# Kernel tuning notes

Measured on AMD Instinct MI355X. Metric: run time of the kernel, lower is better.

## Reference

```python
import jax, jax.numpy as jnp
import numpy as np

H = 16
DH = 64


def _apply_rotary(x, cos, sin):
    # x: [b, h, s, d]; cos/sin: [s, d//2] -> broadcast to [1, 1, s, d//2]
    x1 = x[..., ::2]
    x2 = x[..., 1::2]
    c = cos[None, None]
    s = sin[None, None]
    rot = jnp.stack([x1 * c - x2 * s, x1 * s + x2 * c], axis=-1)
    return rot.reshape(x.shape)


def setup_inputs() -> dict:
    key = jax.random.key(0)
    ks = jax.random.split(key, 7)
    dim = 1024
    std = 0.02
    x = jax.random.normal(ks[0], (2, 2048, dim), dtype=jnp.float32)
    persistent = jax.random.normal(ks[1], (2, 16, dim), dtype=jnp.float32)
    memory = jax.random.normal(ks[2], (2, 64, dim), dtype=jnp.float32)
    Wq = jax.random.normal(ks[3], (dim, dim), dtype=jnp.float32) * std
    Wk = jax.random.normal(ks[4], (dim, dim), dtype=jnp.float32) * std
    Wv = jax.random.normal(ks[5], (dim, dim), dtype=jnp.float32) * std
    Wo = jax.random.normal(ks[6], (dim, dim), dtype=jnp.float32) * std
    return {"x": x, "persistent": persistent, "memory": memory,
            "Wq": Wq, "Wk": Wk, "Wv": Wv, "Wo": Wo}


def reference(x, persistent, memory, Wq, Wk, Wv, Wo):
    b, L, dim = x.shape
    P = persistent.shape[1] + memory.shape[1]  # prefix_len
    full_x = jnp.concatenate([persistent, memory, x], axis=1)  # [b, P+L, dim]
    S = full_x.shape[1]
    scale = DH ** -0.5

    def proj(W):
        y = full_x @ W.T  # [b, S, dim]
        return y.reshape(b, S, H, DH).transpose(0, 2, 1, 3)  # [b, H, S, DH]

    q = proj(Wq)
    k = proj(Wk)
    v = proj(Wv)

    # RoPE only on the main (input) segment, positions starting at 0.
    pos = jnp.arange(L, dtype=jnp.float32)
    inv_freq = 1.0 / (10000.0 ** (jnp.arange(0, DH, 2, dtype=jnp.float32) / DH))
    freqs = pos[:, None] * inv_freq[None, :]  # [L, DH//2]
    cos, sin = jnp.cos(freqs), jnp.sin(freqs)

    q_main = _apply_rotary(q[:, :, P:], cos, sin)  # [b, H, L, DH]
    k = jnp.concatenate([k[:, :, :P], _apply_rotary(k[:, :, P:], cos, sin)], axis=2)

    # Only main-segment query rows affect the returned output (output[:, P:]).
    # Mask for main queries: prefix keys fully visible; causal within main.
    qi = jnp.arange(L)[:, None]
    kj = jnp.arange(S)[None, :]
    mask = (kj < P) | ((kj - P) <= qi)  # [L, S]

    scores = jnp.einsum('bhqd,bhkd->bhqk', q_main, k) * scale  # [b, H, L, S]
    scores = jnp.where(mask[None, None], scores, -jnp.inf)
    attn = jax.nn.softmax(scores, axis=-1)
    out = jnp.einsum('bhqk,bhkd->bhqd', attn, v)  # [b, H, L, DH]
    out = out.transpose(0, 2, 1, 3).reshape(b, L, dim)
    return out @ Wo.T
```

## Files before the change

### kernel.cpp

```cpp
#include <hip/hip_runtime.h>
#include <math.h>

#define BB    2
#define LL    2048
#define DIM   1024
#define NH    16
#define DHD   64
#define NPER  16
#define NMEM  64
#define PFX   80
#define SS    2128
#define MQKV  (BB*SS)
#define NQKV  3072
#define MOUT  (BB*LL)

typedef __attribute__((ext_vector_type(4)))  float f32x4;
typedef __attribute__((ext_vector_type(16))) float f32x16;
typedef __attribute__((ext_vector_type(8)))  short bf16x8;
typedef unsigned short u16;
typedef unsigned int   u32;

union I4B8 { int4 i; bf16x8 v; };

__device__ __forceinline__ u16 f2bf(float x) {
    union { float f; u32 u; } v; v.f = x;
    return (u16)((v.u + 0x7fffu + ((v.u >> 16) & 1u)) >> 16);
}
__device__ __forceinline__ u32 cvtpk(float lo, float hi) {
    u32 r; asm("v_cvt_pk_bf16_f32 %0, %1, %2" : "=v"(r) : "v"(lo), "v"(hi));
    return r;
}
__device__ __forceinline__ void gload_lds16(const void* g, void* l) {
    __builtin_amdgcn_global_load_lds(
        (__attribute__((address_space(1))) void*)(g),
        (__attribute__((address_space(3))) void*)(l), 16, 0, 0);
}

__global__ __launch_bounds__(256)
void prep_kernel(const float* __restrict__ x,  const float* __restrict__ pe,
                 const float* __restrict__ me, const float* __restrict__ Wq,
                 const float* __restrict__ Wk, const float* __restrict__ Wv,
                 const float* __restrict__ Wo,
                 u16* __restrict__ xbf, u16* __restrict__ wqkv,
                 u16* __restrict__ wobf,
                 float* __restrict__ ropeC, float* __restrict__ ropeS)
{
    const int nthr = gridDim.x * blockDim.x;
    const int t0   = blockIdx.x * blockDim.x + threadIdx.x;

    for (int g = t0; g < MQKV * (DIM / 4); g += nthr) {
        int d4  = g & 255;
        int row = g >> 8;
        int b   = row >= SS;
        int s   = row - b * SS;
        const float* src;
        if (s < NPER)     src = pe + ((size_t)(b * NPER + s)) * DIM;
        else if (s < PFX) src = me + ((size_t)(b * NMEM + (s - NPER))) * DIM;
        else              src = x  + ((size_t)(b * LL   + (s - PFX)))  * DIM;
        float4 v = *reinterpret_cast<const float4*>(src + d4 * 4);
        ushort4 o; o.x = f2bf(v.x); o.y = f2bf(v.y); o.z = f2bf(v.z); o.w = f2bf(v.w);
        *reinterpret_cast<ushort4*>(xbf + (size_t)g * 4) = o;
    }
    for (int g = t0; g < NQKV * (DIM / 4); g += nthr) {
        int row = g >> 8;
        const float* src = (row < 1024) ? (Wq + (size_t)row * DIM)
                         : (row < 2048) ? (Wk + (size_t)(row - 1024) * DIM)
                         :                (Wv + (size_t)(row - 2048) * DIM);
        float4 v = *reinterpret_cast<const float4*>(src + (g & 255) * 4);
        ushort4 o; o.x = f2bf(v.x); o.y = f2bf(v.y); o.z = f2bf(v.z); o.w = f2bf(v.w);
        *reinterpret_cast<ushort4*>(wqkv + (size_t)g * 4) = o;
    }
    for (int g = t0; g < DIM * (DIM / 4); g += nthr) {
        float4 v = *reinterpret_cast<const float4*>(Wo + (size_t)g * 4);
        ushort4 o; o.x = f2bf(v.x); o.y = f2bf(v.y); o.z = f2bf(v.z); o.w = f2bf(v.w);
        *reinterpret_cast<ushort4*>(wobf + (size_t)g * 4) = o;
    }
    for (int i = t0; i < LL * 32; i += nthr) {
        int pos = i >> 5, fi = i & 31;
        float ang = (float)pos * exp2f(-(float)fi * 0.41524101186092029f);
        ropeC[i] = cosf(ang);
        ropeS[i] = sinf(ang);
    }
}

template <int MODE>
__global__ __launch_bounds__(256)
void mfma_gemm(const u16* __restrict__ A, const u16* __restrict__ Bw,
               const float* __restrict__ ropeC, const float* __restrict__ ropeS,
               u16* __restrict__ qb, u16* __restrict__ kb,
               u16* __restrict__ vb, float* __restrict__ outp)
{
    __shared__ short As[128 * 32] __attribute__((aligned(16)));
    __shared__ short Bs[128 * 32] __attribute__((aligned(16)));

    const int tid  = threadIdx.x;
    const int lane = tid & 63;
    const int wid  = tid >> 6;
    const int wr   = wid >> 1, wc = wid & 1;
    const int bm   = blockIdx.x * 128;
    const int bn   = blockIdx.y * 128;
    const int Mtot = (MODE == 0) ? MQKV : MOUT;

    f32x4 acc[4][4];
#pragma unroll
    for (int m = 0; m < 4; ++m)
#pragma unroll
        for (int n = 0; n < 4; ++n) acc[m][n] = (f32x4)(0.f);

    const int r0 = wid * 32 + (lane >> 2);
    const int cc = (lane & 3) * 8;

    for (int k0 = 0; k0 < DIM; k0 += 32) {
        int ra0 = bm + r0;      if (ra0 > Mtot - 1) ra0 = Mtot - 1;
        int ra1 = bm + r0 + 16; if (ra1 > Mtot - 1) ra1 = Mtot - 1;
        gload_lds16(A + (size_t)ra0 * DIM + k0 + cc, As + wid * 1024);
        gload_lds16(A + (size_t)ra1 * DIM + k0 + cc, As + wid * 1024 + 512);
        int rb0 = bn + r0, rb1 = bn + r0 + 16;
        gload_lds16(Bw + (size_t)rb0 * DIM + k0 + cc, Bs + wid * 1024);
        gload_lds16(Bw + (size_t)rb1 * DIM + k0 + cc, Bs + wid * 1024 + 512);
        __syncthreads();

        bf16x8 wf[4], xf[4];
#pragma unroll
        for (int m = 0; m < 4; ++m)
            wf[m] = *reinterpret_cast<const bf16x8*>(
                Bs + (wr * 64 + m * 16 + (lane & 15)) * 32 + (lane >> 4) * 8);
#pragma unroll
        for (int n = 0; n < 4; ++n)
            xf[n] = *reinterpret_cast<const bf16x8*>(
                As + (wc * 64 + n * 16 + (lane & 15)) * 32 + (lane >> 4) * 8);
#pragma unroll
        for (int m = 0; m < 4; ++m)
#pragma unroll
            for (int n = 0; n < 4; ++n)
                acc[m][n] = __builtin_amdgcn_mfma_f32_16x16x32_bf16(
                    wf[m], xf[n], acc[m][n], 0, 0, 0);
        __syncthreads();
    }

    const int cbase = bn + wr * 64 + ((lane >> 4) << 2);
    const int rbase = bm + wc * 64 + (lane & 15);
    const int which = bn >> 10;

#pragma unroll
    for (int n = 0; n < 4; ++n) {
        const int row = rbase + n * 16;
        if (row >= Mtot) continue;
        const int b = row >= SS;
        const int s = row - b * SS;
#pragma unroll
        for (int m = 0; m < 4; ++m) {
            const int c0 = cbase + m * 16;
            float v0 = acc[m][n][0], v1 = acc[m][n][1];
            float v2 = acc[m][n][2], v3 = acc[m][n][3];
            if (MODE == 1) {
                *reinterpret_cast<float4*>(&outp[(size_t)row * DIM + c0]) =
                    make_float4(v0, v1, v2, v3);
            } else {
                const int nn = c0 & 1023;
                const int h  = nn >> 6;
                const int dh = nn & 63;
                if (which != 2 && s >= PFX) {
                    const int pos = s - PFX;
                    float2 cs = *reinterpret_cast<const float2*>(ropeC + pos * 32 + (dh >> 1));
                    float2 sn = *reinterpret_cast<const float2*>(ropeS + pos * 32 + (dh >> 1));
                    float t0 = v0 * cs.x - v1 * sn.x;
                    v1 = v0 * sn.x + v1 * cs.x; v0 = t0;
                    float t2 = v2 * cs.y - v3 * sn.y;
                    v3 = v2 * sn.y + v3 * cs.y; v2 = t2;
                }
                ushort4 o;
                o.x = f2bf(v0); o.y = f2bf(v1); o.z = f2bf(v2); o.w = f2bf(v3);
                if (which == 0) {
                    if (s >= PFX)
                        *reinterpret_cast<ushort4*>(
                            &qb[(((size_t)b * NH + h) * LL + (s - PFX)) * DHD + dh]) = o;
                } else if (which == 1) {
                    *reinterpret_cast<ushort4*>(
                        &kb[(((size_t)b * NH + h) * SS + s) * DHD + dh]) = o;
                } else {
                    *reinterpret_cast<ushort4*>(
                        &vb[(((size_t)b * NH + h) * SS + s) * DHD + dh]) = o;
                }
            }
        }
    }
}

__device__ __forceinline__ void attn_load_tile(
    const u16* __restrict__ kb0, const u16* __restrict__ vb0,
    int j0, int tid, int vp, int vo,
    int4& k0r, int4& k1r, int4& v0r, int4& v1r)
{
    int key0 = tid >> 3,        o0 = tid & 7;
    int c1   = tid + 256;
    int key1 = c1 >> 3,         o1 = c1 & 7;
    int jg0 = j0 + key0; if (jg0 > SS - 1) jg0 = SS - 1;
    int jg1 = j0 + key1; if (jg1 > SS - 1) jg1 = SS - 1;
    k0r = *reinterpret_cast<const int4*>(kb0 + (size_t)jg0 * DHD + o0 * 8);
    k1r = *reinterpret_cast<const int4*>(kb0 + (size_t)jg1 * DHD + o1 * 8);
    int ja  = j0 + 2 * vp;     if (ja  > SS - 1) ja  = SS - 1;
    int jb2 = j0 + 2 * vp + 1; if (jb2 > SS - 1) jb2 = SS - 1;
    v0r = *reinterpret_cast<const int4*>(vb0 + (size_t)ja  * DHD + vo * 8);
    v1r = *reinterpret_cast<const int4*>(vb0 + (size_t)jb2 * DHD + vo * 8);
}

__global__ __launch_bounds__(256, 2)
void attn_mfma(const u16* __restrict__ qb, const u16* __restrict__ kb,
               const u16* __restrict__ vb, u16* __restrict__ ctx)
{
    __shared__ u16 Ks[64 * 64] __attribute__((aligned(16)));
    __shared__ u16 Vt[64 * 64] __attribute__((aligned(16)));
    __shared__ u16 Ot[4][32 * 72] __attribute__((aligned(16)));

    const int tid  = threadIdx.x;
    const int lane = tid & 63;
    const int wv   = tid >> 6;
    const int h    = lane >> 5;
    const int ql   = lane & 31;

    const int bh   = blockIdx.y;
    const int b    = bh >> 4;
    const int head = bh & 15;
    int qt = blockIdx.x;
    if (b) qt = 15 - qt;
    const int q0  = qt * 128;
    const int q0w = q0 + 32 * wv;

    const u16* qrow = qb + ((size_t)bh * LL + q0w + ql) * DHD;
    bf16x8 qf[4];
#pragma unroll
    for (int ks = 0; ks < 4; ++ks) {
        I4B8 t; t.i = *reinterpret_cast<const int4*>(qrow + ks * 16 + h * 8);
        qf[ks] = t.v;
    }

    f32x16 oa0 = (f32x16)(0.f), oa1 = (f32x16)(0.f);
    float m = -INFINITY, l = 0.f;

    const u16* kb0 = kb + (size_t)bh * SS * DHD;
    const u16* vb0 = vb + (size_t)bh * SS * DHD;

    const int ntiles   = (PFX + q0 + 128 + 63) / 64;
    const int wave_lim = PFX + q0w + 31;
    const int vp = tid & 31;
    const int vo = tid >> 5;

    int4 rk0, rk1, rv0, rv1;
    attn_load_tile(kb0, vb0, 0, tid, vp, vo, rk0, rk1, rv0, rv1);

    for (int kt = 0; kt < ntiles; ++kt) {
        const int j0 = kt * 64;

        {
            int key0 = tid >> 3, o0 = tid & 7;
            int c1 = tid + 256;
            int key1 = c1 >> 3, o1 = c1 & 7;
            *reinterpret_cast<int4*>((char*)Ks + ((key0 * 128 + o0 * 16) ^ ((key0 & 7) << 4))) = rk0;
            *reinterpret_cast<int4*>((char*)Ks + ((key1 * 128 + o1 * 16) ^ ((key1 & 7) << 4))) = rk1;
            const u16* pa = reinterpret_cast<const u16*>(&rv0);
            const u16* pb = reinterpret_cast<const u16*>(&rv1);
#pragma unroll
            for (int d = 0; d < 8; ++d) {
                u32 wpk = (u32)pa[d] | ((u32)pb[d] << 16);
                int dh = vo * 8 + d;
                *reinterpret_cast<u32*>((char*)Vt + ((dh * 128 + vp * 4) ^ ((d & 7) << 4))) = wpk;
            }
        }
        __syncthreads();

        int4 nk0, nk1, nv0, nv1;
        attn_load_tile(kb0, vb0, j0 + 64, tid, vp, vo, nk0, nk1, nv0, nv1);

        if (j0 <= wave_lim) {
            f32x16 s0 = (f32x16)(0.f), s1 = (f32x16)(0.f);
            __builtin_amdgcn_s_setprio(1);
#pragma unroll
            for (int ks = 0; ks < 4; ++ks) {
                I4B8 k0, k1;
                k0.i = *reinterpret_cast<const int4*>(
                    (const char*)Ks + (((ql) * 128 + ks * 32 + h * 16) ^ ((ql & 7) << 4)));
                k1.i = *reinterpret_cast<const int4*>(
                    (const char*)Ks + (((32 + ql) * 128 + ks * 32 + h * 16) ^ ((ql & 7) << 4)));
                s0 = __builtin_amdgcn_mfma_f32_32x32x16_bf16(k0.v, qf[ks], s0, 0, 0, 0);
                s1 = __builtin_amdgcn_mfma_f32_32x32x16_bf16(k1.v, qf[ks], s1, 0, 0, 0);
            }
            __builtin_amdgcn_s_setprio(0);
            float sv[32];
#pragma unroll
            for (int i = 0; i < 16; ++i) { sv[i] = s0[i] * 0.125f; sv[16 + i] = s1[i] * 0.125f; }
            if (j0 + 63 > PFX + q0w) {
                const int lim = PFX + q0w + ql - j0;
#pragma unroll
                for (int i = 0; i < 32; ++i) {
                    int koff = ((i >= 16) ? 32 : 0) + (i & 3) + 8 * ((i & 15) >> 2) + 4 * h;
                    if (koff > lim) sv[i] = -INFINITY;
                }
            }
            float mt = sv[0];
#pragma unroll
            for (int i = 1; i < 32; ++i) mt = fmaxf(mt, sv[i]);
            mt = fmaxf(mt, __shfl_xor(mt, 32));
            float mn = fmaxf(m, mt);
            float f = __expf(m - mn);
            m = mn;
            float ls = 0.f;
            u32 W0[8], W1[8];
#pragma unroll
            for (int i = 0; i < 8; ++i) {
                float pa = __expf(sv[2 * i] - m);
                float pb = __expf(sv[2 * i + 1] - m);
                ls += pa + pb;
                W0[i] = cvtpk(pa, pb);
            }
#pragma unroll
            for (int i = 0; i < 8; ++i) {
                float pa = __expf(sv[16 + 2 * i] - m);
                float pb = __expf(sv[16 + 2 * i + 1] - m);
                ls += pa + pb;
                W1[i] = cvtpk(pa, pb);
            }
            ls += __shfl_xor(ls, 32);
            l = l * f + ls;
#pragma unroll
            for (int i = 0; i < 16; ++i) { oa0[i] *= f; oa1[i] *= f; }

            __builtin_amdgcn_s_setprio(1);
#pragma unroll
            for (int ks = 0; ks < 4; ++ks) {
                const int a4 = (ks & 1) * 4;
                u32 A0, A1, A2, A3;
                if (ks < 2) { A0 = W0[a4]; A1 = W0[a4 + 1]; A2 = W0[a4 + 2]; A3 = W0[a4 + 3]; }
                else        { A0 = W1[a4]; A1 = W1[a4 + 1]; A2 = W1[a4 + 2]; A3 = W1[a4 + 3]; }
                asm volatile("v_permlane32_swap_b32 %0, %1" : "+v"(A0), "+v"(A2));
                asm volatile("v_permlane32_swap_b32 %0, %1" : "+v"(A1), "+v"(A3));
                I4B8 pf; pf.i = make_int4((int)A0, (int)A1, (int)A2, (int)A3);
                I4B8 vf0, vf1;
                vf0.i = *reinterpret_cast<const int4*>(
                    (const char*)Vt + (((ql) * 128 + ks * 32 + h * 16) ^ ((ql & 7) << 4)));
                vf1.i = *reinterpret_cast<const int4*>(
                    (const char*)Vt + (((32 + ql) * 128 + ks * 32 + h * 16) ^ ((ql & 7) << 4)));
                oa0 = __builtin_amdgcn_mfma_f32_32x32x16_bf16(vf0.v, pf.v, oa0, 0, 0, 0);
                oa1 = __builtin_amdgcn_mfma_f32_32x32x16_bf16(vf1.v, pf.v, oa1, 0, 0, 0);
            }
            __builtin_amdgcn_s_setprio(0);
        }
        __syncthreads();
        rk0 = nk0; rk1 = nk1; rv0 = nv0; rv1 = nv1;
    }

    const float inv = 1.f / l;
    u16* orow = &Ot[wv][ql * 72];
#pragma unroll
    for (int i = 0; i < 8; ++i) {
        u32 w0 = cvtpk(oa0[2 * i] * inv, oa0[2 * i + 1] * inv);
        u32 w1 = cvtpk(oa1[2 * i] * inv, oa1[2 * i + 1] * inv);
        int dh0 = ((2 * i) & 3) + 8 * ((2 * i) >> 2) + 4 * h;
        *reinterpret_cast<u32*>(&orow[dh0]) = w0;
        *reinterpret_cast<u32*>(&orow[32 + dh0]) = w1;
    }
    const int rr = lane >> 1, hh = lane & 1;
    const u16* src = &Ot[wv][rr * 72 + hh * 32];
    u16* dst = ctx + ((size_t)(b * LL + q0 + 32 * wv + rr)) * DIM + head * DHD + hh * 32;
#pragma unroll
    for (int i = 0; i < 4; ++i) {
        int4 t = *reinterpret_cast<const int4*>(src + i * 8);
        *reinterpret_cast<int4*>(dst + i * 8) = t;
    }
}

extern "C" void kernel_launch(void* const* d_in, const int* in_sizes, int n_in,
                              void* d_out, int out_size, void* d_ws, size_t ws_size,
                              hipStream_t stream)
{
    const float* x  = (const float*)d_in[0];
    const float* pe = (const float*)d_in[1];
    const float* me = (const float*)d_in[2];
    const float* Wq = (const float*)d_in[3];
    const float* Wk = (const float*)d_in[4];
    const float* Wv = (const float*)d_in[5];
    const float* Wo = (const float*)d_in[6];
    float* out = (float*)d_out;

    u16* xbf  = (u16*)d_ws;
    u16* wqkv = xbf + (size_t)MQKV * DIM;
    u16* wobf = wqkv + (size_t)NQKV * DIM;
    float* ropeC = (float*)(wobf + (size_t)DIM * DIM);
    float* ropeS = ropeC + LL * 32;
    u16* qbf = (u16*)(ropeS + LL * 32);
    u16* kbf = qbf + (size_t)BB * NH * LL * DHD;
    u16* vbf = kbf + (size_t)BB * NH * SS * DHD;
    u16* ctx = vbf + (size_t)BB * NH * SS * DHD;

    hipLaunchKernelGGL(prep_kernel, dim3(2048), dim3(256), 0, stream,
                       x, pe, me, Wq, Wk, Wv, Wo, xbf, wqkv, wobf, ropeC, ropeS);
    hipLaunchKernelGGL((mfma_gemm<0>), dim3((MQKV + 127) / 128, NQKV / 128), dim3(256), 0, stream,
                       xbf, wqkv, ropeC, ropeS, qbf, kbf, vbf, nullptr);
    hipLaunchKernelGGL(attn_mfma, dim3(16, BB * NH), dim3(256), 0, stream,
                       qbf, kbf, vbf, ctx);
    hipLaunchKernelGGL((mfma_gemm<1>), dim3(MOUT / 128, DIM / 128), dim3(256), 0, stream,
                       ctx, wobf, nullptr, nullptr, nullptr, nullptr, nullptr, out);
}
```

Before: 153.1 us.

## Replace QKV GEMM with 256x256 double-buffered, swizzled 8-wave MFMA kernel

Result: no change. 151.8 us (-0.9%).

```diff
diff --git a/kernel.cpp b/kernel.cpp
--- a/kernel.cpp
+++ b/kernel.cpp
@@ -36,6 +36,9 @@
         (__attribute__((address_space(3))) void*)(l), 16, 0, 0);
 }
 
+#define BARRIER()  asm volatile("s_barrier" ::: "memory")
+#define VMCNT8()   asm volatile("s_waitcnt vmcnt(8)" ::: "memory")
+
 __global__ __launch_bounds__(256)
 void prep_kernel(const float* __restrict__ x,  const float* __restrict__ pe,
                  const float* __restrict__ me, const float* __restrict__ Wq,
@@ -83,12 +86,205 @@
     }
 }
 
-template <int MODE>
+__device__ __forceinline__ void stage_half8(const u16* __restrict__ src, int grow0,
+                                            int rmax, int k0, short* ldsbase, int tid)
+{
+#pragma unroll
+    for (int rr = 0; rr < 2; ++rr) {
+        int t   = tid + rr * 512;
+        int row = t >> 3;
+        int c   = t & 7;
+        int g = grow0 + row; if (g > rmax) g = rmax;
+        gload_lds16(src + (size_t)g * DIM + k0 + ((c ^ (row & 7)) << 3),
+                    ldsbase + (tid >> 6) * 512 + rr * 4096);
+    }
+}
+
+__device__ __forceinline__ bf16x8 ldsfrag(const short* hb, int row, int kbyte)
+{
+    int byte = (row * 128 + kbyte) ^ ((row & 7) << 4);
+    I4B8 t;
+    t.i = *reinterpret_cast<const int4*>(reinterpret_cast<const char*>(hb) + byte);
+    return t.v;
+}
+
+__global__ __launch_bounds__(512, 2)
+void qkv_gemm8(const u16* __restrict__ X, const u16* __restrict__ Wq3,
+               const float* __restrict__ ropeC, const float* __restrict__ ropeS,
+               u16* __restrict__ qb, u16* __restrict__ kb, u16* __restrict__ vb)
+{
+    __shared__ short Xs[2][16384] __attribute__((aligned(16)));
+    __shared__ short Ws[2][16384] __attribute__((aligned(16)));
+
+    const int tid  = threadIdx.x;
+    const int lane = tid & 63;
+    const int wid  = tid >> 6;
+    const int wm   = wid >> 2;
+    const int wn   = wid & 3;
+    const int bm   = blockIdx.x * 256;
+    const int bn   = blockIdx.y * 256;
+
+    f32x4 acc[8][4];
+#pragma unroll
+    for (int r = 0; r < 8; ++r)
+#pragma unroll
+        for (int c = 0; c < 4; ++c) acc[r][c] = (f32x4)(0.f);
+
+    stage_half8(X,   bm,       MQKV - 1, 0,  &Xs[0][0],    tid);
+    stage_half8(X,   bm + 128, MQKV - 1, 0,  &Xs[0][8192], tid);
+    stage_half8(Wq3, bn,       NQKV - 1, 0,  &Ws[0][0],    tid);
+    stage_half8(Wq3, bn + 128, NQKV - 1, 0,  &Ws[0][8192], tid);
+    stage_half8(X,   bm,       MQKV - 1, 64, &Xs[1][0],    tid);
+    stage_half8(X,   bm + 128, MQKV - 1, 64, &Xs[1][8192], tid);
+    stage_half8(Wq3, bn,       NQKV - 1, 64, &Ws[1][0],    tid);
+    stage_half8(Wq3, bn + 128, NQKV - 1, 64, &Ws[1][8192], tid);
+    VMCNT8();
+    BARRIER();
+
+    const int frow = lane & 15;
+    const int fkb  = (lane >> 4) * 16;
+    const int wrow = (wn & 1) * 64;
+    const short* XhA[2] = { &Xs[0][0] + wm * 8192,        &Xs[1][0] + wm * 8192 };
+    const short* WhA[2] = { &Ws[0][0] + (wn >> 1) * 8192, &Ws[1][0] + (wn >> 1) * 8192 };
+
+    for (int it = 0; it < 8; ++it) {
+        int ksA = it * 128 + 128; if (ksA >= 1024) ksA = 0;
+        int ksB = it * 128 + 192; if (ksB >= 1024) ksB = 64;
+#pragma unroll
+        for (int sub = 0; sub < 2; ++sub) {
+            const short* Xh = XhA[sub];
+            const short* Wh = WhA[sub];
+            const int kst = sub ? ksB : ksA;
+            short* XsN = &Xs[sub][0];
+            short* WsN = &Ws[sub][0];
+            bf16x8 xfA[4][2], xfB[4][2], wfA[2][2], wfB[2][2];
+
+#pragma unroll
+            for (int r = 0; r < 4; ++r)
+#pragma unroll
+                for (int ks = 0; ks < 2; ++ks)
+                    xfA[r][ks] = ldsfrag(Xh, r * 16 + frow, ks * 64 + fkb);
+#pragma unroll
+            for (int c = 0; c < 2; ++c)
+#pragma unroll
+                for (int ks = 0; ks < 2; ++ks)
+                    wfA[c][ks] = ldsfrag(Wh, wrow + c * 16 + frow, ks * 64 + fkb);
+            BARRIER();
+            __builtin_amdgcn_s_setprio(1);
+#pragma unroll
+            for (int r = 0; r < 4; ++r)
+#pragma unroll
+                for (int c = 0; c < 2; ++c)
+#pragma unroll
+                    for (int ks = 0; ks < 2; ++ks)
+                        acc[r][c] = __builtin_amdgcn_mfma_f32_16x16x32_bf16(
+                            wfA[c][ks], xfA[r][ks], acc[r][c], 0, 0, 0);
+            __builtin_amdgcn_s_setprio(0);
+            BARRIER();
+
+#pragma unroll
+            for (int c = 0; c < 2; ++c)
+#pragma unroll
+                for (int ks = 0; ks < 2; ++ks)
+                    wfB[c][ks] = ldsfrag(Wh, wrow + 32 + c * 16 + frow, ks * 64 + fkb);
+            BARRIER();
+            __builtin_amdgcn_s_setprio(1);
+#pragma unroll
+            for (int r = 0; r < 4; ++r)
+#pragma unroll
+                for (int c = 0; c < 2; ++c)
+#pragma unroll
+                    for (int ks = 0; ks < 2; ++ks)
+                        acc[r][c + 2] = __builtin_amdgcn_mfma_f32_16x16x32_bf16(
+                            wfB[c][ks], xfA[r][ks], acc[r][c + 2], 0, 0, 0);
+            __builtin_amdgcn_s_setprio(0);
+            BARRIER();
+
+#pragma unroll
+            for (int r = 0; r < 4; ++r)
+#pragma unroll
+                for (int ks = 0; ks < 2; ++ks)
+                    xfB[r][ks] = ldsfrag(Xh, 64 + r * 16 + frow, ks * 64 + fkb);
+            stage_half8(Wq3, bn,       NQKV - 1, kst, WsN,        tid);
+            stage_half8(Wq3, bn + 128, NQKV - 1, kst, WsN + 8192, tid);
+            BARRIER();
+            __builtin_amdgcn_s_setprio(1);
+#pragma unroll
+            for (int r = 0; r < 4; ++r)
+#pragma unroll
+                for (int c = 0; c < 2; ++c)
+#pragma unroll
+                    for (int ks = 0; ks < 2; ++ks)
+                        acc[r + 4][c] = __builtin_amdgcn_mfma_f32_16x16x32_bf16(
+                            wfA[c][ks], xfB[r][ks], acc[r + 4][c], 0, 0, 0);
+            __builtin_amdgcn_s_setprio(0);
+            BARRIER();
+
+            stage_half8(X, bm,       MQKV - 1, kst, XsN,        tid);
+            stage_half8(X, bm + 128, MQKV - 1, kst, XsN + 8192, tid);
+            BARRIER();
+            __builtin_amdgcn_s_setprio(1);
+#pragma unroll
+            for (int r = 0; r < 4; ++r)
+#pragma unroll
+                for (int c = 0; c < 2; ++c)
+#pragma unroll
+                    for (int ks = 0; ks < 2; ++ks)
+                        acc[r + 4][c + 2] = __builtin_amdgcn_mfma_f32_16x16x32_bf16(
+                            wfB[c][ks], xfB[r][ks], acc[r + 4][c + 2], 0, 0, 0);
+            __builtin_amdgcn_s_setprio(0);
+            VMCNT8();
+            BARRIER();
+        }
+    }
+
+    const int cbase = bn + wn * 64 + ((lane >> 4) << 2);
+    const int rbase = bm + wm * 128 + (lane & 15);
+    const int which = bn >> 10;
+
+#pragma unroll
+    for (int xr = 0; xr < 8; ++xr) {
+        const int row = rbase + xr * 16;
+        if (row >= MQKV) continue;
+        const int b = row >= SS;
+        const int s = row - b * SS;
+#pragma unroll
+        for (int wc = 0; wc < 4; ++wc) {
+            const int c0 = cbase + wc * 16;
+            float v0 = acc[xr][wc][0], v1 = acc[xr][wc][1];
+            float v2 = acc[xr][wc][2], v3 = acc[xr][wc][3];
+            const int nn = c0 & 1023;
+            const int h  = nn >> 6;
+            const int dh = nn & 63;
+            if (which != 2 && s >= PFX) {
+                const int pos = s - PFX;
+                float2 cs = *reinterpret_cast<const float2*>(ropeC + pos * 32 + (dh >> 1));
+                float2 sn = *reinterpret_cast<const float2*>(ropeS + pos * 32 + (dh >> 1));
+                float t0 = v0 * cs.x - v1 * sn.x;
+                v1 = v0 * sn.x + v1 * cs.x; v0 = t0;
+                float t2 = v2 * cs.y - v3 * sn.y;
+                v3 = v2 * sn.y + v3 * cs.y; v2 = t2;
+            }
+            ushort4 o;
+            o.x = f2bf(v0); o.y = f2bf(v1); o.z = f2bf(v2); o.w = f2bf(v3);
+            if (which == 0) {
+                if (s >= PFX)
+                    *reinterpret_cast<ushort4*>(
+                        &qb[(((size_t)b * NH + h) * LL + (s - PFX)) * DHD + dh]) = o;
+            } else if (which == 1) {
+                *reinterpret_cast<ushort4*>(
+                    &kb[(((size_t)b * NH + h) * SS + s) * DHD + dh]) = o;
+            } else {
+                *reinterpret_cast<ushort4*>(
+                    &vb[(((size_t)b * NH + h) * SS + s) * DHD + dh]) = o;
+            }
+        }
+    }
+}
+
 __global__ __launch_bounds__(256)
-void mfma_gemm(const u16* __restrict__ A, const u16* __restrict__ Bw,
-               const float* __restrict__ ropeC, const float* __restrict__ ropeS,
-               u16* __restrict__ qb, u16* __restrict__ kb,
-               u16* __restrict__ vb, float* __restrict__ outp)
+void wo_gemm(const u16* __restrict__ A, const u16* __restrict__ Bw,
+             float* __restrict__ outp)
 {
     __shared__ short As[128 * 32] __attribute__((aligned(16)));
     __shared__ short Bs[128 * 32] __attribute__((aligned(16)));
@@ -99,7 +295,6 @@
     const int wr   = wid >> 1, wc = wid & 1;
     const int bm   = blockIdx.x * 128;
     const int bn   = blockIdx.y * 128;
-    const int Mtot = (MODE == 0) ? MQKV : MOUT;
 
     f32x4 acc[4][4];
 #pragma unroll
@@ -111,13 +306,10 @@
     const int cc = (lane & 3) * 8;
 
     for (int k0 = 0; k0 < DIM; k0 += 32) {
-        int ra0 = bm + r0;      if (ra0 > Mtot - 1) ra0 = Mtot - 1;
-        int ra1 = bm + r0 + 16; if (ra1 > Mtot - 1) ra1 = Mtot - 1;
-        gload_lds16(A + (size_t)ra0 * DIM + k0 + cc, As + wid * 1024);
-        gload_lds16(A + (size_t)ra1 * DIM + k0 + cc, As + wid * 1024 + 512);
-        int rb0 = bn + r0, rb1 = bn + r0 + 16;
-        gload_lds16(Bw + (size_t)rb0 * DIM + k0 + cc, Bs + wid * 1024);
-        gload_lds16(Bw + (size_t)rb1 * DIM + k0 + cc, Bs + wid * 1024 + 512);
+        gload_lds16(A + (size_t)(bm + r0) * DIM + k0 + cc, As + wid * 1024);
+        gload_lds16(A + (size_t)(bm + r0 + 16) * DIM + k0 + cc, As + wid * 1024 + 512);
+        gload_lds16(Bw + (size_t)(bn + r0) * DIM + k0 + cc, Bs + wid * 1024);
+        gload_lds16(Bw + (size_t)(bn + r0 + 16) * DIM + k0 + cc, Bs + wid * 1024 + 512);
         __syncthreads();
 
         bf16x8 wf[4], xf[4];
@@ -140,49 +332,14 @@
 
     const int cbase = bn + wr * 64 + ((lane >> 4) << 2);
     const int rbase = bm + wc * 64 + (lane & 15);
-    const int which = bn >> 10;
-
 #pragma unroll
     for (int n = 0; n < 4; ++n) {
         const int row = rbase + n * 16;
-        if (row >= Mtot) continue;
-        const int b = row >= SS;
-        const int s = row - b * SS;
 #pragma unroll
         for (int m = 0; m < 4; ++m) {
             const int c0 = cbase + m * 16;
-            float v0 = acc[m][n][0], v1 = acc[m][n][1];
-            float v2 = acc[m][n][2], v3 = acc[m][n][3];
-            if (MODE == 1) {
-                *reinterpret_cast<float4*>(&outp[(size_t)row * DIM + c0]) =
-                    make_float4(v0, v1, v2, v3);
-            } else {
-                const int nn = c0 & 1023;
-                const int h  = nn >> 6;
-                const int dh = nn & 63;
-                if (which != 2 && s >= PFX) {
-                    const int pos = s - PFX;
-                    float2 cs = *reinterpret_cast<const float2*>(ropeC + pos * 32 + (dh >> 1));
-                    float2 sn = *reinterpret_cast<const float2*>(ropeS + pos * 32 + (dh >> 1));
-                    float t0 = v0 * cs.x - v1 * sn.x;
-                    v1 = v0 * sn.x + v1 * cs.x; v0 = t0;
-                    float t2 = v2 * cs.y - v3 * sn.y;
-                    v3 = v2 * sn.y + v3 * cs.y; v2 = t2;
-                }
-                ushort4 o;
-                o.x = f2bf(v0); o.y = f2bf(v1); o.z = f2bf(v2); o.w = f2bf(v3);
-                if (which == 0) {
-                    if (s >= PFX)
-                        *reinterpret_cast<ushort4*>(
-                            &qb[(((size_t)b * NH + h) * LL + (s - PFX)) * DHD + dh]) = o;
-                } else if (which == 1) {
-                    *reinterpret_cast<ushort4*>(
-                        &kb[(((size_t)b * NH + h) * SS + s) * DHD + dh]) = o;
-                } else {
-                    *reinterpret_cast<ushort4*>(
-                        &vb[(((size_t)b * NH + h) * SS + s) * DHD + dh]) = o;
-                }
-            }
+            *reinterpret_cast<float4*>(&outp[(size_t)row * DIM + c0]) =
+                make_float4(acc[m][n][0], acc[m][n][1], acc[m][n][2], acc[m][n][3]);
         }
     }
 }
@@ -394,10 +551,10 @@
 
     hipLaunchKernelGGL(prep_kernel, dim3(2048), dim3(256), 0, stream,
                        x, pe, me, Wq, Wk, Wv, Wo, xbf, wqkv, wobf, ropeC, ropeS);
-    hipLaunchKernelGGL((mfma_gemm<0>), dim3((MQKV + 127) / 128, NQKV / 128), dim3(256), 0, stream,
-                       xbf, wqkv, ropeC, ropeS, qbf, kbf, vbf, nullptr);
+    hipLaunchKernelGGL(qkv_gemm8, dim3((MQKV + 255) / 256, NQKV / 256), dim3(512), 0, stream,
+                       xbf, wqkv, ropeC, ropeS, qbf, kbf, vbf);
     hipLaunchKernelGGL(attn_mfma, dim3(16, BB * NH), dim3(256), 0, stream,
                        qbf, kbf, vbf, ctx);
-    hipLaunchKernelGGL((mfma_gemm<1>), dim3(MOUT / 128, DIM / 128), dim3(256), 0, stream,
-                       ctx, wobf, nullptr, nullptr, nullptr, nullptr, nullptr, out);
-}
+    hipLaunchKernelGGL(wo_gemm, dim3(MOUT / 128, DIM / 128), dim3(256), 0, stream,
+                       ctx, wobf, out);
+}
```

## Double-buffer QKV GEMM with larger tiles and row-major QKV output

Applied to the files above, without the earlier changes.

Result: faster. 136.8 us (-10.7%).

```diff
diff --git a/kernel.cpp b/kernel.cpp
--- a/kernel.cpp
+++ b/kernel.cpp
@@ -36,6 +36,9 @@
         (__attribute__((address_space(3))) void*)(l), 16, 0, 0);
 }
 
+#define BARRIER()  __builtin_amdgcn_s_barrier()
+#define VMCNT0()   asm volatile("s_waitcnt vmcnt(0)")
+
 __global__ __launch_bounds__(256)
 void prep_kernel(const float* __restrict__ x,  const float* __restrict__ pe,
                  const float* __restrict__ me, const float* __restrict__ Wq,
@@ -83,12 +86,118 @@
     }
 }
 
-template <int MODE>
+__global__ __launch_bounds__(256, 2)
+void qkv_gemm2p(const u16* __restrict__ X, const u16* __restrict__ Wq3,
+                const float* __restrict__ ropeC, const float* __restrict__ ropeS,
+                u16* __restrict__ qkvraw)
+{
+    __shared__ short Xs[2][256 * 32] __attribute__((aligned(16)));
+    __shared__ short Ws[2][128 * 32] __attribute__((aligned(16)));
+
+    const int tid  = threadIdx.x;
+    const int lane = tid & 63;
+    const int wid  = tid >> 6;
+    const int bm   = blockIdx.x * 256;
+    const int bn   = blockIdx.y * 128;
+
+    f32x4 acc[4][8];
+#pragma unroll
+    for (int m = 0; m < 4; ++m)
+#pragma unroll
+        for (int n = 0; n < 8; ++n) acc[m][n] = (f32x4)(0.f);
+
+    const int srow = lane >> 2;
+    const int scc  = (lane & 3) * 8;
+
+#define STAGE_XW(buf, k0)                                                      \
+    {                                                                          \
+        _Pragma("unroll")                                                      \
+        for (int it = 0; it < 4; ++it) {                                       \
+            int r = wid * 64 + it * 16 + srow;                                 \
+            int g = bm + r; if (g > MQKV - 1) g = MQKV - 1;                    \
+            gload_lds16(X + (size_t)g * DIM + (k0) + scc,                      \
+                        &Xs[buf][(wid * 64 + it * 16) * 32]);                  \
+        }                                                                      \
+        _Pragma("unroll")                                                      \
+        for (int it = 0; it < 2; ++it) {                                       \
+            int r = wid * 32 + it * 16 + srow;                                 \
+            gload_lds16(Wq3 + (size_t)(bn + r) * DIM + (k0) + scc,             \
+                        &Ws[buf][(wid * 32 + it * 16) * 32]);                  \
+        }                                                                      \
+    }
+
+    STAGE_XW(0, 0);
+    VMCNT0();
+    BARRIER();
+
+    const int frow = lane & 15;
+    const int fkb  = (lane >> 4) * 8;
+
+    for (int t = 0; t < 32; ++t) {
+        const int cur = t & 1;
+        int knext = (t + 1) * 32; if (knext >= DIM) knext = 0;
+        STAGE_XW(cur ^ 1, knext);
+
+        bf16x8 xf[4], wf[8];
+#pragma unroll
+        for (int m = 0; m < 4; ++m)
+            xf[m] = *reinterpret_cast<const bf16x8*>(
+                &Xs[cur][(wid * 64 + m * 16 + frow) * 32 + fkb]);
+#pragma unroll
+        for (int n = 0; n < 8; ++n)
+            wf[n] = *reinterpret_cast<const bf16x8*>(
+                &Ws[cur][(n * 16 + frow) * 32 + fkb]);
+
+        __builtin_amdgcn_s_setprio(1);
+#pragma unroll
+        for (int m = 0; m < 4; ++m)
+#pragma unroll
+            for (int n = 0; n < 8; ++n)
+                acc[m][n] = __builtin_amdgcn_mfma_f32_16x16x32_bf16(
+                    wf[n], xf[m], acc[m][n], 0, 0, 0);
+        __builtin_amdgcn_s_setprio(0);
+
+        VMCNT0();
+        BARRIER();
+    }
+#undef STAGE_XW
+
+    const int cbase = bn + ((lane >> 4) << 2);
+    const int rbase = bm + wid * 64 + (lane & 15);
+    const int which = bn >> 10;
+
+#pragma unroll
+    for (int m = 0; m < 4; ++m) {
+        const int row = rbase + m * 16;
+        if (row >= MQKV) continue;
+        const int b = row >= SS;
+        const int s = row - b * SS;
+        const bool rope = (which != 2) && (s >= PFX);
+        const int pos = s - PFX;
+#pragma unroll
+        for (int n = 0; n < 8; ++n) {
+            const int c0 = cbase + n * 16;
+            float v0 = acc[m][n][0], v1 = acc[m][n][1];
+            float v2 = acc[m][n][2], v3 = acc[m][n][3];
+            if (rope) {
+                const int dh = c0 & 63;
+                float2 cs = *reinterpret_cast<const float2*>(ropeC + pos * 32 + (dh >> 1));
+                float2 sn = *reinterpret_cast<const float2*>(ropeS + pos * 32 + (dh >> 1));
+                float t0 = v0 * cs.x - v1 * sn.x;
+                v1 = v0 * sn.x + v1 * cs.x; v0 = t0;
+                float t2 = v2 * cs.y - v3 * sn.y;
+                v3 = v2 * sn.y + v3 * cs.y; v2 = t2;
+            }
+            ushort4 o;
+            o.x = f2bf(v0); o.y = f2bf(v1); o.z = f2bf(v2); o.w = f2bf(v3);
+            *reinterpret_cast<ushort4*>(&qkvraw[(size_t)row * NQKV + c0]) = o;
+        }
+    }
+}
+
 __global__ __launch_bounds__(256)
-void mfma_gemm(const u16* __restrict__ A, const u16* __restrict__ Bw,
-               const float* __restrict__ ropeC, const float* __restrict__ ropeS,
-               u16* __restrict__ qb, u16* __restrict__ kb,
-               u16* __restrict__ vb, float* __restrict__ outp)
+void wo_gemm(const u16* __restrict__ A, const u16* __restrict__ Bw,
+             float* __restrict__ outp)
 {
     __shared__ short As[128 * 32] __attribute__((aligned(16)));
     __shared__ short Bs[128 * 32] __attribute__((aligned(16)));
@@ -99,7 +208,6 @@
     const int wr   = wid >> 1, wc = wid & 1;
     const int bm   = blockIdx.x * 128;
     const int bn   = blockIdx.y * 128;
-    const int Mtot = (MODE == 0) ? MQKV : MOUT;
 
     f32x4 acc[4][4];
 #pragma unroll
@@ -111,13 +219,10 @@
     const int cc = (lane & 3) * 8;
 
     for (int k0 = 0; k0 < DIM; k0 += 32) {
-        int ra0 = bm + r0;      if (ra0 > Mtot - 1) ra0 = Mtot - 1;
-        int ra1 = bm + r0 + 16; if (ra1 > Mtot - 1) ra1 = Mtot - 1;
-        gload_lds16(A + (size_t)ra0 * DIM + k0 + cc, As + wid * 1024);
-        gload_lds16(A + (size_t)ra1 * DIM + k0 + cc, As + wid * 1024 + 512);
-        int rb0 = bn + r0, rb1 = bn + r0 + 16;
-        gload_lds16(Bw + (size_t)rb0 * DIM + k0 + cc, Bs + wid * 1024);
-        gload_lds16(Bw + (size_t)rb1 * DIM + k0 + cc, Bs + wid * 1024 + 512);
+        gload_lds16(A + (size_t)(bm + r0) * DIM + k0 + cc, As + wid * 1024);
+        gload_lds16(A + (size_t)(bm + r0 + 16) * DIM + k0 + cc, As + wid * 1024 + 512);
+        gload_lds16(Bw + (size_t)(bn + r0) * DIM + k0 + cc, Bs + wid * 1024);
+        gload_lds16(Bw + (size_t)(bn + r0 + 16) * DIM + k0 + cc, Bs + wid * 1024 + 512);
         __syncthreads();
 
         bf16x8 wf[4], xf[4];
@@ -140,49 +245,14 @@
 
     const int cbase = bn + wr * 64 + ((lane >> 4) << 2);
     const int rbase = bm + wc * 64 + (lane & 15);
-    const int which = bn >> 10;
-
 #pragma unroll
     for (int n = 0; n < 4; ++n) {
         const int row = rbase + n * 16;
-        if (row >= Mtot) continue;
-        const int b = row >= SS;
-        const int s = row - b * SS;
 #pragma unroll
         for (int m = 0; m < 4; ++m) {
             const int c0 = cbase + m * 16;
-            float v0 = acc[m][n][0], v1 = acc[m][n][1];
-            float v2 = acc[m][n][2], v3 = acc[m][n][3];
-            if (MODE == 1) {
-                *reinterpret_cast<float4*>(&outp[(size_t)row * DIM + c0]) =
-                    make_float4(v0, v1, v2, v3);
-            } else {
-                const int nn = c0 & 1023;
-                const int h  = nn >> 6;
-                const int dh = nn & 63;
-                if (which != 2 && s >= PFX) {
-                    const int pos = s - PFX;
-                    float2 cs = *reinterpret_cast<const float2*>(ropeC + pos * 32 + (dh >> 1));
-                    float2 sn = *reinterpret_cast<const float2*>(ropeS + pos * 32 + (dh >> 1));
-                    float t0 = v0 * cs.x - v1 * sn.x;
-                    v1 = v0 * sn.x + v1 * cs.x; v0 = t0;
-                    float t2 = v2 * cs.y - v3 * sn.y;
-                    v3 = v2 * sn.y + v3 * cs.y; v2 = t2;
-                }
-                ushort4 o;
-                o.x = f2bf(v0); o.y = f2bf(v1); o.z = f2bf(v2); o.w = f2bf(v3);
-                if (which == 0) {
-                    if (s >= PFX)
-                        *reinterpret_cast<ushort4*>(
-                            &qb[(((size_t)b * NH + h) * LL + (s - PFX)) * DHD + dh]) = o;
-                } else if (which == 1) {
-                    *reinterpret_cast<ushort4*>(
-                        &kb[(((size_t)b * NH + h) * SS + s) * DHD + dh]) = o;
-                } else {
-                    *reinterpret_cast<ushort4*>(
-                        &vb[(((size_t)b * NH + h) * SS + s) * DHD + dh]) = o;
-                }
-            }
+            *reinterpret_cast<float4*>(&outp[(size_t)row * DIM + c0]) =
+                make_float4(acc[m][n][0], acc[m][n][1], acc[m][n][2], acc[m][n][3]);
         }
     }
 }
@@ -197,17 +267,16 @@
     int key1 = c1 >> 3,         o1 = c1 & 7;
     int jg0 = j0 + key0; if (jg0 > SS - 1) jg0 = SS - 1;
     int jg1 = j0 + key1; if (jg1 > SS - 1) jg1 = SS - 1;
-    k0r = *reinterpret_cast<const int4*>(kb0 + (size_t)jg0 * DHD + o0 * 8);
-    k1r = *reinterpret_cast<const int4*>(kb0 + (size_t)jg1 * DHD + o1 * 8);
+    k0r = *reinterpret_cast<const int4*>(kb0 + (size_t)jg0 * NQKV + o0 * 8);
+    k1r = *reinterpret_cast<const int4*>(kb0 + (size_t)jg1 * NQKV + o1 * 8);
     int ja  = j0 + 2 * vp;     if (ja  > SS - 1) ja  = SS - 1;
     int jb2 = j0 + 2 * vp + 1; if (jb2 > SS - 1) jb2 = SS - 1;
-    v0r = *reinterpret_cast<const int4*>(vb0 + (size_t)ja  * DHD + vo * 8);
-    v1r = *reinterpret_cast<const int4*>(vb0 + (size_t)jb2 * DHD + vo * 8);
+    v0r = *reinterpret_cast<const int4*>(vb0 + (size_t)ja  * NQKV + vo * 8);
+    v1r = *reinterpret_cast<const int4*>(vb0 + (size_t)jb2 * NQKV + vo * 8);
 }
 
 __global__ __launch_bounds__(256, 2)
-void attn_mfma(const u16* __restrict__ qb, const u16* __restrict__ kb,
-               const u16* __restrict__ vb, u16* __restrict__ ctx)
+void attn_mfma(const u16* __restrict__ qkvraw, u16* __restrict__ ctx)
 {
     __shared__ u16 Ks[64 * 64] __attribute__((aligned(16)));
     __shared__ u16 Vt[64 * 64] __attribute__((aligned(16)));
@@ -227,7 +296,7 @@
     const int q0  = qt * 128;
     const int q0w = q0 + 32 * wv;
 
-    const u16* qrow = qb + ((size_t)bh * LL + q0w + ql) * DHD;
+    const u16* qrow = qkvraw + (size_t)(b * SS + PFX + q0w + ql) * NQKV + head * DHD;
     bf16x8 qf[4];
 #pragma unroll
     for (int ks = 0; ks < 4; ++ks) {
@@ -238,8 +307,8 @@
     f32x16 oa0 = (f32x16)(0.f), oa1 = (f32x16)(0.f);
     float m = -INFINITY, l = 0.f;
 
-    const u16* kb0 = kb + (size_t)bh * SS * DHD;
-    const u16* vb0 = vb + (size_t)bh * SS * DHD;
+    const u16* kb0 = qkvraw + (size_t)b * SS * NQKV + 1024 + head * DHD;
+    const u16* vb0 = qkvraw + (size_t)b * SS * NQKV + 2048 + head * DHD;
 
     const int ntiles   = (PFX + q0 + 128 + 63) / 64;
     const int wave_lim = PFX + q0w + 31;
@@ -387,17 +456,15 @@
     u16* wobf = wqkv + (size_t)NQKV * DIM;
     float* ropeC = (float*)(wobf + (size_t)DIM * DIM);
     float* ropeS = ropeC + LL * 32;
-    u16* qbf = (u16*)(ropeS + LL * 32);
-    u16* kbf = qbf + (size_t)BB * NH * LL * DHD;
-    u16* vbf = kbf + (size_t)BB * NH * SS * DHD;
-    u16* ctx = vbf + (size_t)BB * NH * SS * DHD;
+    u16* qkvraw = (u16*)(ropeS + LL * 32);
+    u16* ctx = qkvraw + (size_t)MQKV * NQKV;
 
     hipLaunchKernelGGL(prep_kernel, dim3(2048), dim3(256), 0, stream,
                        x, pe, me, Wq, Wk, Wv, Wo, xbf, wqkv, wobf, ropeC, ropeS);
-    hipLaunchKernelGGL((mfma_gemm<0>), dim3((MQKV + 127) / 128, NQKV / 128), dim3(256), 0, stream,
-                       xbf, wqkv, ropeC, ropeS, qbf, kbf, vbf, nullptr);
+    hipLaunchKernelGGL(qkv_gemm2p, dim3((MQKV + 255) / 256, NQKV / 128), dim3(256), 0, stream,
+                       xbf, wqkv, ropeC, ropeS, qkvraw);
     hipLaunchKernelGGL(attn_mfma, dim3(16, BB * NH), dim3(256), 0, stream,
-                       qbf, kbf, vbf, ctx);
-    hipLaunchKernelGGL((mfma_gemm<1>), dim3(MOUT / 128, DIM / 128), dim3(256), 0, stream,
-                       ctx, wobf, nullptr, nullptr, nullptr, nullptr, nullptr, out);
-}
+                       qkvraw, ctx);
+    hipLaunchKernelGGL(wo_gemm, dim3(MOUT / 128, DIM / 128), dim3(256), 0, stream,
+                       ctx, wobf, out);
+}
```
